# Kernel tuning notes

Hardware: AMD Instinct MI355X
Metric: run time of the kernel (lower is better)

## Reference

```python
import jax, jax.numpy as jnp
import numpy as np

SMOOTH_STEP_PARAM = 1.0  # = 1/gamma in the TEL paper
DEPTH = 6


def smooth_step(x):
    # TEL smooth-step: 0 for u<=-1/2, 1 for u>=1/2, cubic -2u^3+1.5u+0.5 inside.
    u = SMOOTH_STEP_PARAM * x
    inner = (-2.0 * u + 1.5) * u * u + (u + 0.5) * 0.0 + (-2.0 * u ** 3 + 1.5 * u + 0.5)
    # use single clean expression for the cubic
    cubic = -2.0 * u ** 3 + 1.5 * u + 0.5
    return jnp.where(u <= -0.5, 0.0, jnp.where(u >= 0.5, 1.0, cubic))


def setup_inputs() -> dict:
    key = jax.random.key(0)
    k1, k2, k3 = jax.random.split(key, 3)
    B, D, T, O = 32768, 1024, 8, 128
    num_leaves = 2 ** DEPTH
    x = jax.random.normal(k1, (B, D), dtype=jnp.float32)
    # RandomUniform(-0.01, 0.01) initializers in the original layer
    node_weights = jax.random.uniform(k2, (T, D, num_leaves - 1), dtype=jnp.float32,
                                      minval=-0.01, maxval=0.01)
    leaf_weights = jax.random.uniform(k3, (T, O, num_leaves), dtype=jnp.float32,
                                      minval=-0.01, maxval=0.01)
    return {"x": x, "node_weights": node_weights, "leaf_weights": leaf_weights}


def reference(x, node_weights, leaf_weights):
    B = x.shape[0]
    T = node_weights.shape[0]
    # routing probabilities at every internal node (BFS order): [B, T, 2^depth-1]
    s = smooth_step(jnp.einsum('bd,tdi->bti', x, node_weights))
    # accumulate leaf reach probabilities level by level (left child gets s)
    mu = jnp.ones((B, T, 1), dtype=x.dtype)
    start = 0
    for level in range(DEPTH):
        width = 2 ** level
        s_lvl = s[:, :, start:start + width]           # [B, T, width]
        mu = jnp.stack([mu * s_lvl, mu * (1.0 - s_lvl)], axis=-1)
        mu = mu.reshape(B, T, 2 * width)
        start += width
    # weighted sum of leaf vectors, summed over trees (sum_outputs=True)
    return jnp.einsum('btl,tol->bo', mu, leaf_weights)
```

## Files before the change

### kernel.cpp

```cpp
#include <hip/hip_runtime.h>
#include <hip/hip_bf16.h>
#include <stdint.h>

#define KDIM 1024
#define XSTR2 520
#define TSTR 72
#define RSTR 584

typedef __attribute__((ext_vector_type(4))) float f32x4;
typedef __attribute__((ext_vector_type(8))) short bf16x8;

#define WS_LB_OFF ((size_t)1 << 20)

__device__ __forceinline__ unsigned short f2bf_rne(float f) {
    unsigned u = __float_as_uint(f);
    u = (u + 0x7fffu + ((u >> 16) & 1u)) >> 16;
    return (unsigned short)u;
}

__device__ __forceinline__ unsigned int pack2_bf16(float a, float b) {
    __hip_bfloat162 h = __float22bfloat162_rn(make_float2(a, b));
    union { __hip_bfloat162 h; unsigned int u; } cv;
    cv.h = h;
    return cv.u;
}

__device__ __forceinline__ float gs_get(const uint4* q, int i) {
    uint4 v = q[i >> 3];
    int c = (i >> 1) & 3;
    unsigned w = (c == 0) ? v.x : (c == 1) ? v.y : (c == 2) ? v.z : v.w;
    return __uint_as_float((i & 1) ? (w & 0xffff0000u) : (w << 16));
}

__global__ void prep(const float* __restrict__ nw, const float* __restrict__ lw,
                     unsigned short* __restrict__ wb, unsigned short* __restrict__ lb) {
    int b = blockIdx.x;
    if (b < 2048) {
        int idx = b * 256 + threadIdx.x;
        int e    = idx & 7;
        int lane = (idx >> 3) & 63;
        int cb   = (idx >> 9) & 31;
        int ks   = idx >> 14;
        int col = cb * 16 + (lane & 15);
        int k   = ks * 32 + (lane >> 4) * 8 + e;
        int t = col >> 6, i = col & 63;
        float v = (i < 63) ? nw[(t * KDIM + k) * 63 + i] : 0.0f;
        wb[idx] = f2bf_rne(v);
    } else {
        int idx = (b - 2048) * 256 + threadIdx.x;
        int e    = idx & 7;
        int lane = (idx >> 3) & 63;
        int obk  = (idx >> 9) & 7;
        int kq   = idx >> 12;
        int o = obk * 16 + (lane & 15);
        int c = kq * 32 + (lane >> 4) * 8 + e;
        int t = c >> 6, l = c & 63;
        lb[idx] = f2bf_rne(lw[(t * 128 + o) * 64 + l]);
    }
}

__device__ __forceinline__ void compute_half(const unsigned short* __restrict__ xb,
                                             const unsigned short* __restrict__ wb0,
                                             int ksbase, int l16, int quad,
                                             f32x4 (&acc)[2][4]) {
    #pragma unroll 4
    for (int ksl = 0; ksl < 16; ++ksl) {
        const int ks = ksbase + ksl;
        bf16x8 bf[4], af[2];
        #pragma unroll
        for (int rt = 0; rt < 4; ++rt)
            bf[rt] = *(const bf16x8*)&xb[(rt * 16 + l16) * XSTR2 + ksl * 32 + quad * 8];
        const unsigned short* wbase = wb0 + (size_t)ks * 16384;
        af[0] = *(const bf16x8*)(wbase);
        af[1] = *(const bf16x8*)(wbase + 512);
        #pragma unroll
        for (int ct = 0; ct < 2; ++ct)
            #pragma unroll
            for (int rt = 0; rt < 4; ++rt)
                acc[ct][rt] = __builtin_amdgcn_mfma_f32_16x16x32_bf16(af[ct], bf[rt], acc[ct][rt], 0, 0, 0);
    }
}

__launch_bounds__(1024, 4)
__global__ void fused(const float* __restrict__ x, const unsigned short* __restrict__ wb,
                      const unsigned short* __restrict__ lb, float* __restrict__ out) {
    __shared__ union __align__(16) {
        unsigned short xs[2][64 * XSTR2];
        unsigned short st[64 * RSTR];
    } sm;

    const int tid  = threadIdx.x;
    const int wave = tid >> 6, lane = tid & 63;
    const int quad = lane >> 4, l16 = lane & 15;
    const int mb   = blockIdx.x;

    f32x4 acc[2][4];
    const f32x4 z4 = {0.f, 0.f, 0.f, 0.f};
    #pragma unroll
    for (int a = 0; a < 2; ++a)
        #pragma unroll
        for (int b = 0; b < 4; ++b) acc[a][b] = z4;

    const int srow = tid >> 4, sf4 = tid & 15;
    const float* xgr = x + (size_t)(mb * 64 + srow) * KDIM;
    const unsigned short* wb0 = wb + ((size_t)(wave * 2) * 64 + lane) * 8;

    #pragma unroll
    for (int seg = 0; seg < 8; ++seg) {
        int f4 = sf4 + seg * 16;
        f32x4 v = __builtin_nontemporal_load((const f32x4*)(xgr + f4 * 4));
        uint2 pk;
        pk.x = pack2_bf16(v[0], v[1]);
        pk.y = pack2_bf16(v[2], v[3]);
        *(uint2*)&sm.xs[0][srow * XSTR2 + f4 * 4] = pk;
    }
    __syncthreads();

    f32x4 pre[8];
    #pragma unroll
    for (int seg = 0; seg < 8; ++seg) {
        int f4 = sf4 + seg * 16;
        pre[seg] = __builtin_nontemporal_load((const f32x4*)(xgr + 512 + f4 * 4));
    }

    compute_half(sm.xs[0], wb0, 0, l16, quad, acc);

    #pragma unroll
    for (int seg = 0; seg < 8; ++seg) {
        int f4 = sf4 + seg * 16;
        uint2 pk;
        pk.x = pack2_bf16(pre[seg][0], pre[seg][1]);
        pk.y = pack2_bf16(pre[seg][2], pre[seg][3]);
        *(uint2*)&sm.xs[1][srow * XSTR2 + f4 * 4] = pk;
    }
    __syncthreads();

    compute_half(sm.xs[1], wb0, 16, l16, quad, acc);

    __syncthreads();
    #pragma unroll
    for (int rt = 0; rt < 4; ++rt) {
        int r = rt * 16 + l16;
        #pragma unroll
        for (int ct = 0; ct < 2; ++ct) {
            int colb = wave * 32 + ct * 16 + quad * 4;
            f32x4 a = acc[ct][rt];
            float s0[4];
            #pragma unroll
            for (int j = 0; j < 4; ++j) {
                float u = a[j];
                u = fminf(fmaxf(u, -0.5f), 0.5f);
                s0[j] = u * (1.5f - 2.0f * u * u) + 0.5f;
            }
            uint2 pk;
            pk.x = pack2_bf16(s0[0], s0[1]);
            pk.y = pack2_bf16(s0[2], s0[3]);
            *(uint2*)&sm.st[r * RSTR + (colb >> 6) * TSTR + (colb & 63)] = pk;
        }
    }
    __syncthreads();
    if (tid < 512) {
        int r = tid >> 3, t = tid & 7;
        unsigned short* base = &sm.st[r * RSTR + t * TSTR];
        uint4 q[8];
        #pragma unroll
        for (int c = 0; c < 8; ++c) q[c] = *(const uint4*)(base + c * 8);
        float mu[32];
        mu[0] = 1.0f;
        int start = 0;
        #pragma unroll
        for (int lvl = 0; lvl < 5; ++lvl) {
            int width = 1 << lvl;
            #pragma unroll
            for (int j = width - 1; j >= 0; --j) {
                float m = mu[j], s_ = gs_get(q, start + j);
                mu[2 * j + 1] = m * (1.0f - s_);
                mu[2 * j]     = m * s_;
            }
            start += width;
        }
        #pragma unroll
        for (int c = 0; c < 8; ++c) {
            unsigned pk2[4];
            #pragma unroll
            for (int e = 0; e < 4; ++e) {
                int j = c * 4 + e;
                float m = mu[j], s_ = gs_get(q, 31 + j);
                pk2[e] = pack2_bf16(m * s_, m * (1.0f - s_));
            }
            uint4 v; v.x = pk2[0]; v.y = pk2[1]; v.z = pk2[2]; v.w = pk2[3];
            *(uint4*)(base + c * 8) = v;
        }
    }
    __syncthreads();
    {
        int rtile = wave & 3, obk2 = wave >> 2;
        int mr = rtile * 16 + l16;
        f32x4 a2[2];
        a2[0] = z4; a2[1] = z4;
        #pragma unroll
        for (int kq = 0; kq < 16; ++kq) {
            int c0 = kq * 32 + quad * 8;
            bf16x8 bmu = *(const bf16x8*)&sm.st[mr * RSTR + (c0 >> 6) * TSTR + (c0 & 63)];
            #pragma unroll
            for (int i = 0; i < 2; ++i) {
                int obk = obk2 * 2 + i;
                bf16x8 alf = *(const bf16x8*)(lb + ((size_t)((kq * 8 + obk) * 64 + lane)) * 8);
                a2[i] = __builtin_amdgcn_mfma_f32_16x16x32_bf16(alf, bmu, a2[i], 0, 0, 0);
            }
        }
        int rowg = mb * 64 + rtile * 16 + l16;
        #pragma unroll
        for (int i = 0; i < 2; ++i) {
            int og = (obk2 * 2 + i) * 16 + quad * 4;
            __builtin_nontemporal_store(a2[i], (f32x4*)(out + (size_t)rowg * 128 + og));
        }
    }
}

extern "C" void kernel_launch(void* const* d_in, const int* in_sizes, int n_in,
                              void* d_out, int out_size, void* d_ws, size_t ws_size,
                              hipStream_t stream) {
    const float* x  = (const float*)d_in[0];
    const float* nw = (const float*)d_in[1];
    const float* lw = (const float*)d_in[2];
    float* out = (float*)d_out;

    unsigned short* wb = (unsigned short*)d_ws;
    unsigned short* lb = (unsigned short*)((char*)d_ws + WS_LB_OFF);

    prep<<<2304, 256, 0, stream>>>(nw, lw, wb, lb);
    fused<<<512, 1024, 0, stream>>>(x, wb, lb, out);
}
```

Baseline: 231.3 us.

## Pipeline x staging in eight 128-column chunks with LDS double buffering

Result: no change. 233.0 us (+0.7%).

```diff
diff --git a/kernel.cpp b/kernel.cpp
--- a/kernel.cpp
+++ b/kernel.cpp
@@ -3,7 +3,7 @@
 #include <stdint.h>
 
 #define KDIM 1024
-#define XSTR2 520
+#define XCH 136
 #define TSTR 72
 #define RSTR 584
 
@@ -59,33 +59,11 @@
     }
 }
 
-__device__ __forceinline__ void compute_half(const unsigned short* __restrict__ xb,
-                                             const unsigned short* __restrict__ wb0,
-                                             int ksbase, int l16, int quad,
-                                             f32x4 (&acc)[2][4]) {
-    #pragma unroll 4
-    for (int ksl = 0; ksl < 16; ++ksl) {
-        const int ks = ksbase + ksl;
-        bf16x8 bf[4], af[2];
-        #pragma unroll
-        for (int rt = 0; rt < 4; ++rt)
-            bf[rt] = *(const bf16x8*)&xb[(rt * 16 + l16) * XSTR2 + ksl * 32 + quad * 8];
-        const unsigned short* wbase = wb0 + (size_t)ks * 16384;
-        af[0] = *(const bf16x8*)(wbase);
-        af[1] = *(const bf16x8*)(wbase + 512);
-        #pragma unroll
-        for (int ct = 0; ct < 2; ++ct)
-            #pragma unroll
-            for (int rt = 0; rt < 4; ++rt)
-                acc[ct][rt] = __builtin_amdgcn_mfma_f32_16x16x32_bf16(af[ct], bf[rt], acc[ct][rt], 0, 0, 0);
-    }
-}
-
 __launch_bounds__(1024, 4)
 __global__ void fused(const float* __restrict__ x, const unsigned short* __restrict__ wb,
                       const unsigned short* __restrict__ lb, float* __restrict__ out) {
     __shared__ union __align__(16) {
-        unsigned short xs[2][64 * XSTR2];
+        struct { unsigned short A[64 * XCH], B[64 * XCH]; } xs;
         unsigned short st[64 * RSTR];
     } sm;
 
@@ -101,41 +79,50 @@
         #pragma unroll
         for (int b = 0; b < 4; ++b) acc[a][b] = z4;
 
-    const int srow = tid >> 4, sf4 = tid & 15;
-    const float* xgr = x + (size_t)(mb * 64 + srow) * KDIM;
+    const int srow = tid >> 4, sseg = tid & 15;
+    const float* xgr = x + (size_t)(mb * 64 + srow) * KDIM + sseg * 8;
     const unsigned short* wb0 = wb + ((size_t)(wave * 2) * 64 + lane) * 8;
 
-    #pragma unroll
-    for (int seg = 0; seg < 8; ++seg) {
-        int f4 = sf4 + seg * 16;
-        f32x4 v = __builtin_nontemporal_load((const f32x4*)(xgr + f4 * 4));
-        uint2 pk;
-        pk.x = pack2_bf16(v[0], v[1]);
-        pk.y = pack2_bf16(v[2], v[3]);
-        *(uint2*)&sm.xs[0][srow * XSTR2 + f4 * 4] = pk;
-    }
-    __syncthreads();
-
-    f32x4 pre[8];
-    #pragma unroll
-    for (int seg = 0; seg < 8; ++seg) {
-        int f4 = sf4 + seg * 16;
-        pre[seg] = __builtin_nontemporal_load((const f32x4*)(xgr + 512 + f4 * 4));
-    }
-
-    compute_half(sm.xs[0], wb0, 0, l16, quad, acc);
-
-    #pragma unroll
-    for (int seg = 0; seg < 8; ++seg) {
-        int f4 = sf4 + seg * 16;
-        uint2 pk;
-        pk.x = pack2_bf16(pre[seg][0], pre[seg][1]);
-        pk.y = pack2_bf16(pre[seg][2], pre[seg][3]);
-        *(uint2*)&sm.xs[1][srow * XSTR2 + f4 * 4] = pk;
-    }
-    __syncthreads();
-
-    compute_half(sm.xs[1], wb0, 16, l16, quad, acc);
+    f32x4 p0, p1;
+    auto PRE = [&](int c) {
+        p0 = __builtin_nontemporal_load((const f32x4*)(xgr + c * 128));
+        p1 = __builtin_nontemporal_load((const f32x4*)(xgr + c * 128 + 4));
+    };
+    auto WR = [&](unsigned short* buf) {
+        uint4 pk;
+        pk.x = pack2_bf16(p0[0], p0[1]);
+        pk.y = pack2_bf16(p0[2], p0[3]);
+        pk.z = pack2_bf16(p1[0], p1[1]);
+        pk.w = pack2_bf16(p1[2], p1[3]);
+        *(uint4*)&buf[srow * XCH + sseg * 8] = pk;
+    };
+    auto COMPUTE = [&](const unsigned short* buf, int c) {
+        #pragma unroll
+        for (int ksl = 0; ksl < 4; ++ksl) {
+            bf16x8 bf[4], af[2];
+            #pragma unroll
+            for (int rt = 0; rt < 4; ++rt)
+                bf[rt] = *(const bf16x8*)&buf[(rt * 16 + l16) * XCH + ksl * 32 + quad * 8];
+            const unsigned short* wbase = wb0 + (size_t)(c * 4 + ksl) * 16384;
+            af[0] = *(const bf16x8*)(wbase);
+            af[1] = *(const bf16x8*)(wbase + 512);
+            #pragma unroll
+            for (int ct = 0; ct < 2; ++ct)
+                #pragma unroll
+                for (int rt = 0; rt < 4; ++rt)
+                    acc[ct][rt] = __builtin_amdgcn_mfma_f32_16x16x32_bf16(af[ct], bf[rt], acc[ct][rt], 0, 0, 0);
+        }
+    };
+
+    PRE(0); WR(sm.xs.A); __syncthreads();
+    PRE(1); COMPUTE(sm.xs.A, 0); WR(sm.xs.B); __syncthreads();
+    PRE(2); COMPUTE(sm.xs.B, 1); WR(sm.xs.A); __syncthreads();
+    PRE(3); COMPUTE(sm.xs.A, 2); WR(sm.xs.B); __syncthreads();
+    PRE(4); COMPUTE(sm.xs.B, 3); WR(sm.xs.A); __syncthreads();
+    PRE(5); COMPUTE(sm.xs.A, 4); WR(sm.xs.B); __syncthreads();
+    PRE(6); COMPUTE(sm.xs.B, 5); WR(sm.xs.A); __syncthreads();
+    PRE(7); COMPUTE(sm.xs.A, 6); WR(sm.xs.B); __syncthreads();
+    COMPUTE(sm.xs.B, 7);
 
     __syncthreads();
     #pragma unroll
```
